# Kernel optimization log

Hardware: AMD Instinct MI355X
Metric: run time of the kernel (lower is better)

The kernel has to match this reference:

```python
import jax, jax.numpy as jnp
import numpy as np
from jax import lax

FILTER_SIZE = 3
C_IN = 128
C_OUT = 256
PAD = 1
STRIDE = 1


def setup_inputs() -> dict:
    key = jax.random.key(0)
    k1, k2 = jax.random.split(key)
    prev_a = jax.random.normal(k1, (32, 56, 56, C_IN), dtype=jnp.float32)
    # filter_w initialized ~ N(0, 1) as in the original tf.random.normal
    filter_w = jax.random.normal(k2, (FILTER_SIZE, FILTER_SIZE, C_IN, C_OUT), dtype=jnp.float32)
    filter_b = jnp.zeros((1, 1, 1, C_OUT), dtype=jnp.float32)
    return {"prev_a": prev_a, "filter_w": filter_w, "filter_b": filter_b}


def reference(prev_a, filter_w, filter_b):
    # NHWC input, HWIO filter -> NHWC output; same math as the nested-loop conv:
    # z[i,h,w,c] = sum(prev_a_pad[i, h*s:h*s+f, w*s:w*s+f, :] * W[:,:,:,c]) + b[c]
    z = lax.conv_general_dilated(
        prev_a,
        filter_w,
        window_strides=(STRIDE, STRIDE),
        padding=[(PAD, PAD), (PAD, PAD)],
        dimension_numbers=("NHWC", "HWIO", "NHWC"),
    )
    z = z + filter_b  # bias broadcast over (m, H, W)
    return jax.nn.relu(z)
```

## Files before the change

### kernel.cpp

```cpp
#include <hip/hip_runtime.h>
#include <hip/hip_bf16.h>


#define NIMG 32
#define HH 56
#define WW 56
#define PH 58
#define PW 58
#define CIN 128
#define COUT 256
#define KTOT 1152
#define PAD_ELEMS (NIMG * PH * PW * CIN)

#define BM 224
#define BK 64
#define NT (KTOT / BK)
#define NBLK ((NIMG * HH * WW) / BM)

#define AREG_SZ 7168
#define BREG_BASE 28672
#define BREG_SZ 8192

typedef __attribute__((ext_vector_type(8))) short bf16x8;
typedef __attribute__((ext_vector_type(4))) short s16x4;
typedef __attribute__((ext_vector_type(4))) float f32x4;

__device__ __forceinline__ short f2bf(float x) {
    union { __hip_bfloat16 b; short s; } u;
    u.b = __float2bfloat16(x);
    return u.s;
}

typedef const void __attribute__((address_space(1)))* gas1_t;
typedef void __attribute__((address_space(3)))* las3_t;
__device__ __forceinline__ void async16(short* lds_p, const short* g) {
    __builtin_amdgcn_global_load_lds((gas1_t)g, (las3_t)lds_p, 16, 0, 0);
}

__global__ __launch_bounds__(256) void pack_input(const float* __restrict__ in,
                                                  short* __restrict__ pad) {
    const int tid  = blockIdx.x * 256 + threadIdx.x;
    const int flat = tid * 8;
    const int c8   = flat & (CIN - 1);
    const int rest = flat >> 7;
    const int iw   = rest % PW;
    const int r2   = rest / PW;
    const int ih   = r2 % PH;
    const int img  = r2 / PH;
    bf16x8 v = (bf16x8)0;
    if (ih >= 1 && ih <= HH && iw >= 1 && iw <= WW) {
        const float* p = in + (((size_t)(img * HH + ih - 1) * WW + (iw - 1)) * CIN + c8);
        const float4 x0 = *(const float4*)p;
        const float4 x1 = *(const float4*)(p + 4);
        v.s0 = f2bf(x0.x); v.s1 = f2bf(x0.y); v.s2 = f2bf(x0.z); v.s3 = f2bf(x0.w);
        v.s4 = f2bf(x1.x); v.s5 = f2bf(x1.y); v.s6 = f2bf(x1.z); v.s7 = f2bf(x1.w);
    }
    *(bf16x8*)(pad + flat) = v;
}

__global__ __launch_bounds__(256) void pack_wgt(const float* __restrict__ w,
                                                short* __restrict__ wt) {
    __shared__ short tile[32][33];
    const int k0 = blockIdx.x * 32;
    const int n0 = blockIdx.y * 32;
    const int t  = threadIdx.x;
    {
        const int kl  = t >> 3;
        const int nl4 = (t & 7) * 4;
        const float4 x = *(const float4*)(w + (size_t)(k0 + kl) * COUT + n0 + nl4);
        tile[kl][nl4 + 0] = f2bf(x.x);
        tile[kl][nl4 + 1] = f2bf(x.y);
        tile[kl][nl4 + 2] = f2bf(x.z);
        tile[kl][nl4 + 3] = f2bf(x.w);
    }
    __syncthreads();
    {
        const int nl  = t >> 3;
        const int kl4 = (t & 7) * 4;
        s16x4 v;
        v.x = tile[kl4 + 0][nl];
        v.y = tile[kl4 + 1][nl];
        v.z = tile[kl4 + 2][nl];
        v.w = tile[kl4 + 3][nl];
        *(s16x4*)(wt + (size_t)(n0 + nl) * KTOT + k0 + kl4) = v;
    }
}

#define FENCE() asm volatile("" ::: "memory")
#define BARRIER() do { FENCE(); __builtin_amdgcn_s_barrier(); FENCE(); } while (0)
#define VMWAIT(N) asm volatile("s_waitcnt vmcnt(" #N ")" ::: "memory")
#define NOSTMT ((void)0)

__global__ __launch_bounds__(512, 2) void conv_mfma(const short* __restrict__ apad,
                                                    const short* __restrict__ bwt,
                                                    const float* __restrict__ bias,
                                                    float* __restrict__ out) {
    __shared__ short lds[61440];

    const int t  = threadIdx.x;
    const int l  = t & 63;
    const int w  = t >> 6;
    const int wm = w >> 2;
    const int wn = w & 3;
    const int fr = l & 15;
    const int fq = l >> 4;

    const int laneoff = fr * 32 + ((fq ^ ((fr >> 1) & 3))) * 8;
    const int afb = wm * 3584;
    const int bfb = wn * 2048;
    const int kcs = (t & 3) ^ ((t >> 3) & 3);

    const int bid = blockIdx.x;
    const int swz = (bid & 7) * (NBLK / 8) + (bid >> 3);
    const int m0  = swz * BM;

    const int r0 = t >> 2;
    int abase0, abase1;
    {
        int m = m0 + r0;
        int img = m / (HH * WW), rem = m - img * (HH * WW);
        int oh = rem / WW, ow = rem - oh * WW;
        abase0 = ((img * PH + oh) * PW + ow) * CIN;
        if (t < 384) {
            m = m0 + r0 + 128;
            img = m / (HH * WW); rem = m - img * (HH * WW);
            oh = rem / WW; ow = rem - oh * WW;
            abase1 = ((img * PH + oh) * PW + ow) * CIN;
        } else {
            abase1 = abase0;
        }
    }
    const int a2lds = (w < 6) ? (4096 + w * 512) : (w * 512);
    const int bbase0 = r0 * KTOT;
    const int bbase1 = (r0 + 128) * KTOT;

    f32x4 acc[7][4];
#pragma unroll
    for (int i = 0; i < 7; ++i)
#pragma unroll
        for (int j = 0; j < 4; ++j) { f32x4 z = {0.f, 0.f, 0.f, 0.f}; acc[i][j] = z; }

    bf16x8 af0[4], af1[3], bf[4];

#define STAGE_A(KT, KH) do {                                                  \
        const int _tap = (KT) >> 1;                                           \
        const int _fh  = (_tap * 11) >> 5;                   \
        const int _fw  = _tap - 3 * _fh;                                      \
        const int _off = (_fh * PW + _fw) * CIN + ((KT) & 1) * 64             \
                         + (KH) * 32 + kcs * 8;                               \
        short* _l = lds + ((((KT) & 1) << 1) + (KH)) * AREG_SZ;               \
        async16(_l + w * 512, apad + abase0 + _off);                          \
        async16(_l + a2lds,   apad + abase1 + _off);                          \
    } while (0)

#define STAGE_B(KT, KH) do {                                                  \
        const int _off = (KT) * 64 + (KH) * 32 + kcs * 8;                     \
        short* _l = lds + BREG_BASE + ((((KT) & 1) << 1) + (KH)) * BREG_SZ;   \
        async16(_l + w * 512,        bwt + bbase0 + _off);                    \
        async16(_l + 4096 + w * 512, bwt + bbase1 + _off);                    \
    } while (0)

#define PH_MH0(BUF, KH, STAGE_STMT, WAIT_STMT) do {                           \
        const short* _a = lds + (((BUF) << 1) + (KH)) * AREG_SZ;              \
        const short* _b = lds + BREG_BASE + (((BUF) << 1) + (KH)) * BREG_SZ;  \
        _Pragma("unroll")                                                     \
        for (int _i = 0; _i < 4; ++_i)                                        \
            af0[_i] = *(const bf16x8*)(_a + afb + _i * 512 + laneoff);        \
        _Pragma("unroll")                                                     \
        for (int _j = 0; _j < 4; ++_j)                                        \
            bf[_j] = *(const bf16x8*)(_b + bfb + _j * 512 + laneoff);         \
        STAGE_STMT;                                                           \
        BARRIER();                                                            \
        __builtin_amdgcn_s_setprio(1);                                        \
        _Pragma("unroll")                                                     \
        for (int _i = 0; _i < 4; ++_i)                                        \
            _Pragma("unroll")                                                 \
            for (int _j = 0; _j < 4; ++_j)                                    \
                acc[_i][_j] = __builtin_amdgcn_mfma_f32_16x16x32_bf16(        \
                    af0[_i], bf[_j], acc[_i][_j], 0, 0, 0);                   \
        __builtin_amdgcn_s_setprio(0);                                        \
        WAIT_STMT;                                                            \
        BARRIER();                                                            \
    } while (0)

#define PH_MH1(BUF, KH, STAGE_STMT, WAIT_STMT) do {                           \
        const short* _a = lds + (((BUF) << 1) + (KH)) * AREG_SZ;              \
        _Pragma("unroll")                                                     \
        for (int _i = 0; _i < 3; ++_i)                                        \
            af1[_i] = *(const bf16x8*)(_a + afb + 2048 + _i * 512 + laneoff); \
        STAGE_STMT;                                                           \
        BARRIER();                                                            \
        __builtin_amdgcn_s_setprio(1);                                        \
        _Pragma("unroll")                                                     \
        for (int _i = 0; _i < 3; ++_i)                                        \
            _Pragma("unroll")                                                 \
            for (int _j = 0; _j < 4; ++_j)                                    \
                acc[4 + _i][_j] = __builtin_amdgcn_mfma_f32_16x16x32_bf16(    \
                    af1[_i], bf[_j], acc[4 + _i][_j], 0, 0, 0);               \
        __builtin_amdgcn_s_setprio(0);                                        \
        WAIT_STMT;                                                            \
        BARRIER();                                                            \
    } while (0)

    STAGE_A(0, 0); STAGE_B(0, 0);
    STAGE_A(0, 1); STAGE_B(0, 1);
    STAGE_A(1, 0); STAGE_B(1, 0);
    VMWAIT(8);
    BARRIER();

#pragma unroll 1
    for (int kt = 0; kt < NT - 2; kt += 2) {
        PH_MH0(0, 0, STAGE_A(kt + 1, 1), NOSTMT);
        PH_MH1(0, 0, STAGE_B(kt + 1, 1), VMWAIT(8));
        PH_MH0(0, 1, STAGE_A(kt + 2, 0), NOSTMT);
        PH_MH1(0, 1, STAGE_B(kt + 2, 0), VMWAIT(8));
        PH_MH0(1, 0, STAGE_A(kt + 2, 1), NOSTMT);
        PH_MH1(1, 0, STAGE_B(kt + 2, 1), VMWAIT(8));
        PH_MH0(1, 1, STAGE_A(kt + 3, 0), NOSTMT);
        PH_MH1(1, 1, STAGE_B(kt + 3, 0), VMWAIT(8));
    }
    PH_MH0(0, 0, STAGE_A(NT - 1, 1), NOSTMT);
    PH_MH1(0, 0, STAGE_B(NT - 1, 1), VMWAIT(8));
    PH_MH0(0, 1, NOSTMT,             NOSTMT);
    PH_MH1(0, 1, NOSTMT,             VMWAIT(4));
    PH_MH0(1, 0, NOSTMT,             NOSTMT);
    PH_MH1(1, 0, NOSTMT,             VMWAIT(0));
    PH_MH0(1, 1, NOSTMT,             NOSTMT);
    PH_MH1(1, 1, NOSTMT,             NOSTMT);

#pragma unroll
    for (int j = 0; j < 4; ++j) {
        const int n  = wn * 64 + j * 16 + fr;
        const float bj = bias[n];
#pragma unroll
        for (int i = 0; i < 7; ++i) {
            const int mr = m0 + wm * 112 + i * 16 + fq * 4;
#pragma unroll
            for (int r = 0; r < 4; ++r) {
                const float v = acc[i][j][r] + bj;
                out[(size_t)(mr + r) * COUT + n] = v > 0.f ? v : 0.f;
            }
        }
    }
#undef STAGE_A
#undef STAGE_B
#undef PH_MH0
#undef PH_MH1
}

extern "C" void kernel_launch(void* const* d_in, const int* in_sizes, int n_in,
                              void* d_out, int out_size, void* d_ws, size_t ws_size,
                              hipStream_t stream) {
    const float* in   = (const float*)d_in[0];
    const float* wgt  = (const float*)d_in[1];
    const float* bias = (const float*)d_in[2];
    float* out = (float*)d_out;

    short* pad = (short*)d_ws;
    short* wt  = (short*)d_ws + PAD_ELEMS;

    pack_input<<<PAD_ELEMS / 8 / 256, 256, 0, stream>>>(in, pad);
    pack_wgt<<<dim3(KTOT / 32, COUT / 32), 256, 0, stream>>>(wgt, wt);

    conv_mfma<<<NBLK, 512, 0, stream>>>(pad, wt, bias, out);
}
```

Before: 199.1 us.

## Double-buffer MFMA fragments to overlap LDS reads with compute, one barrier per phase

Restructures the main loop so the LDS fragment reads for the next phase are issued right after the current phase's MFMAs, using ping-pong register sets (M0a/M0b, M1a/M1b, Ba/Bb). Each phase now needs one barrier instead of two, and the global-load wait counts are retuned. This is meant to hide LDS read latency behind matrix math and halve the barrier count. The cost is more vector registers under the launch bound of 512 threads with 2 blocks, which risks spills or lower occupancy.

```diff
diff --git a/kernel.cpp b/kernel.cpp
--- a/kernel.cpp
+++ b/kernel.cpp
@@ -89,7 +89,6 @@
 #define FENCE() asm volatile("" ::: "memory")
 #define BARRIER() do { FENCE(); __builtin_amdgcn_s_barrier(); FENCE(); } while (0)
 #define VMWAIT(N) asm volatile("s_waitcnt vmcnt(" #N ")" ::: "memory")
-#define NOSTMT ((void)0)
 
 __global__ __launch_bounds__(512, 2) void conv_mfma(const short* __restrict__ apad,
                                                     const short* __restrict__ bwt,
@@ -140,7 +139,7 @@
 #pragma unroll
         for (int j = 0; j < 4; ++j) { f32x4 z = {0.f, 0.f, 0.f, 0.f}; acc[i][j] = z; }
 
-    bf16x8 af0[4], af1[3], bf[4];
+    bf16x8 M0a[4], M0b[4], M1a[3], M1b[3], Ba[4], Bb[4];
 
 #define STAGE_A(KT, KH) do {                                                  \
         const int _tap = (KT) >> 1;                                           \
@@ -160,46 +159,44 @@
         async16(_l + 4096 + w * 512, bwt + bbase1 + _off);                    \
     } while (0)
 
-#define PH_MH0(BUF, KH, STAGE_STMT, WAIT_STMT) do {                           \
-        const short* _a = lds + (((BUF) << 1) + (KH)) * AREG_SZ;              \
-        const short* _b = lds + BREG_BASE + (((BUF) << 1) + (KH)) * BREG_SZ;  \
+#define RD_M0B(M0, BF, REG) do {                                              \
+        const short* _a = lds + (REG) * AREG_SZ;                              \
+        const short* _b = lds + BREG_BASE + (REG) * BREG_SZ;                  \
         _Pragma("unroll")                                                     \
         for (int _i = 0; _i < 4; ++_i)                                        \
-            af0[_i] = *(const bf16x8*)(_a + afb + _i * 512 + laneoff);        \
+            (M0)[_i] = *(const bf16x8*)(_a + afb + _i * 512 + laneoff);       \
         _Pragma("unroll")                                                     \
         for (int _j = 0; _j < 4; ++_j)                                        \
-            bf[_j] = *(const bf16x8*)(_b + bfb + _j * 512 + laneoff);         \
-        STAGE_STMT;                                                           \
-        BARRIER();                                                            \
+            (BF)[_j] = *(const bf16x8*)(_b + bfb + _j * 512 + laneoff);       \
+    } while (0)
+
+#define RD_M1(M1, REG) do {                                                   \
+        const short* _a = lds + (REG) * AREG_SZ;                              \
+        _Pragma("unroll")                                                     \
+        for (int _i = 0; _i < 3; ++_i)                                        \
+            (M1)[_i] = *(const bf16x8*)(_a + afb + 2048 + _i * 512 + laneoff);\
+    } while (0)
+
+#define MM0(M0, BF) do {                                                      \
         __builtin_amdgcn_s_setprio(1);                                        \
         _Pragma("unroll")                                                     \
         for (int _i = 0; _i < 4; ++_i)                                        \
             _Pragma("unroll")                                                 \
             for (int _j = 0; _j < 4; ++_j)                                    \
                 acc[_i][_j] = __builtin_amdgcn_mfma_f32_16x16x32_bf16(        \
-                    af0[_i], bf[_j], acc[_i][_j], 0, 0, 0);                   \
+                    (M0)[_i], (BF)[_j], acc[_i][_j], 0, 0, 0);                \
         __builtin_amdgcn_s_setprio(0);                                        \
-        WAIT_STMT;                                                            \
-        BARRIER();                                                            \
-    } while (0)
-
-#define PH_MH1(BUF, KH, STAGE_STMT, WAIT_STMT) do {                           \
-        const short* _a = lds + (((BUF) << 1) + (KH)) * AREG_SZ;              \
-        _Pragma("unroll")                                                     \
-        for (int _i = 0; _i < 3; ++_i)                                        \
-            af1[_i] = *(const bf16x8*)(_a + afb + 2048 + _i * 512 + laneoff); \
-        STAGE_STMT;                                                           \
-        BARRIER();                                                            \
+    } while (0)
+
+#define MM1(M1, BF) do {                                                      \
         __builtin_amdgcn_s_setprio(1);                                        \
         _Pragma("unroll")                                                     \
         for (int _i = 0; _i < 3; ++_i)                                        \
             _Pragma("unroll")                                                 \
             for (int _j = 0; _j < 4; ++_j)                                    \
                 acc[4 + _i][_j] = __builtin_amdgcn_mfma_f32_16x16x32_bf16(    \
-                    af1[_i], bf[_j], acc[4 + _i][_j], 0, 0, 0);               \
+                    (M1)[_i], (BF)[_j], acc[4 + _i][_j], 0, 0, 0);            \
         __builtin_amdgcn_s_setprio(0);                                        \
-        WAIT_STMT;                                                            \
-        BARRIER();                                                            \
     } while (0)
 
     STAGE_A(0, 0); STAGE_B(0, 0);
@@ -207,26 +204,28 @@
     STAGE_A(1, 0); STAGE_B(1, 0);
     VMWAIT(8);
     BARRIER();
+    RD_M0B(M0a, Ba, 0);
 
 #pragma unroll 1
     for (int kt = 0; kt < NT - 2; kt += 2) {
-        PH_MH0(0, 0, STAGE_A(kt + 1, 1), NOSTMT);
-        PH_MH1(0, 0, STAGE_B(kt + 1, 1), VMWAIT(8));
-        PH_MH0(0, 1, STAGE_A(kt + 2, 0), NOSTMT);
-        PH_MH1(0, 1, STAGE_B(kt + 2, 0), VMWAIT(8));
-        PH_MH0(1, 0, STAGE_A(kt + 2, 1), NOSTMT);
-        PH_MH1(1, 0, STAGE_B(kt + 2, 1), VMWAIT(8));
-        PH_MH0(1, 1, STAGE_A(kt + 3, 0), NOSTMT);
-        PH_MH1(1, 1, STAGE_B(kt + 3, 0), VMWAIT(8));
-    }
-    PH_MH0(0, 0, STAGE_A(NT - 1, 1), NOSTMT);
-    PH_MH1(0, 0, STAGE_B(NT - 1, 1), VMWAIT(8));
-    PH_MH0(0, 1, NOSTMT,             NOSTMT);
-    PH_MH1(0, 1, NOSTMT,             VMWAIT(4));
-    PH_MH0(1, 0, NOSTMT,             NOSTMT);
-    PH_MH1(1, 0, NOSTMT,             VMWAIT(0));
-    PH_MH0(1, 1, NOSTMT,             NOSTMT);
-    PH_MH1(1, 1, NOSTMT,             NOSTMT);
+        STAGE_A(kt + 1, 1); MM0(M0a, Ba); VMWAIT(6); RD_M1(M1a, 0);      BARRIER();
+        STAGE_B(kt + 1, 1); MM1(M1a, Ba);            RD_M0B(M0b, Bb, 1); BARRIER();
+        STAGE_A(kt + 2, 0); MM0(M0b, Bb); VMWAIT(6); RD_M1(M1b, 1);      BARRIER();
+        STAGE_B(kt + 2, 0); MM1(M1b, Bb);            RD_M0B(M0a, Ba, 2); BARRIER();
+        STAGE_A(kt + 2, 1); MM0(M0a, Ba); VMWAIT(6); RD_M1(M1a, 2);      BARRIER();
+        STAGE_B(kt + 2, 1); MM1(M1a, Ba);            RD_M0B(M0b, Bb, 3); BARRIER();
+        STAGE_A(kt + 3, 0); MM0(M0b, Bb); VMWAIT(6); RD_M1(M1b, 3);      BARRIER();
+        STAGE_B(kt + 3, 0); MM1(M1b, Bb);            RD_M0B(M0a, Ba, 0); BARRIER();
+    }
+
+    STAGE_A(NT - 1, 1); MM0(M0a, Ba); VMWAIT(6); RD_M1(M1a, 0);      BARRIER();
+    STAGE_B(NT - 1, 1); MM1(M1a, Ba);            RD_M0B(M0b, Bb, 1); BARRIER();
+    MM0(M0b, Bb); VMWAIT(4); RD_M1(M1b, 1);      BARRIER();
+    MM1(M1b, Bb);            RD_M0B(M0a, Ba, 2); BARRIER();
+    MM0(M0a, Ba); VMWAIT(0); RD_M1(M1a, 2);      BARRIER();
+    MM1(M1a, Ba);            RD_M0B(M0b, Bb, 3); BARRIER();
+    MM0(M0b, Bb);            RD_M1(M1b, 3);      BARRIER();
+    MM1(M1b, Bb);
 
 #pragma unroll
     for (int j = 0; j < 4; ++j) {
@@ -244,8 +243,10 @@
     }
 #undef STAGE_A
 #undef STAGE_B
-#undef PH_MH0
-#undef PH_MH1
+#undef RD_M0B
+#undef RD_M1
+#undef MM0
+#undef MM1
 }
 
 extern "C" void kernel_launch(void* const* d_in, const int* in_sizes, int n_in,
```

Result: no change. 200.6 us (+0.7%).
